# Performance work log

Hardware: AMD Instinct MI355X
Metric: run time of the kernel (lower is better)

## Reference

```python
import jax, jax.numpy as jnp
import numpy as np

IN_FEATURES = 4096
OUT_FEATURES = 11008
W_BITS = 4
GROUP_SIZE = 128
NUM_CHERRIES = 128                       # ceil(4096*0.03125)//8*8
NUM_NORMAL = IN_FEATURES - NUM_CHERRIES  # 3968
N_GROUPS = NUM_NORMAL // GROUP_SIZE      # 31
QROWS = NUM_NORMAL // 8 * W_BITS         # 1984 packed uint8 rows
QMIN = -(2 ** (W_BITS - 1))              # signed int4 min = -8
BATCH = 64


def setup_inputs() -> dict:
    key = jax.random.key(0)
    k1, k2, k3, k4, k5 = jax.random.split(key, 5)
    x = jax.random.normal(k1, (BATCH, IN_FEATURES), jnp.float32)
    # packed 4-bit weights: two nibbles per uint8, stored as [QROWS, out]
    qweight = jax.random.randint(k2, (QROWS, OUT_FEATURES), 0, 256, jnp.int32).astype(jnp.uint8)
    # per-group scales, stored transposed as [n_groups, out]
    scales = jax.random.uniform(k3, (N_GROUPS, OUT_FEATURES), jnp.float32, 0.005, 0.02)
    # full-precision outlier ('cherry') columns, stored as [num_cherries, out]
    cherry_weight = jax.random.normal(k4, (NUM_CHERRIES, OUT_FEATURES), jnp.float32) * 0.02
    rng = np.random.default_rng(0)
    cherry_indices = jnp.asarray(
        np.sort(rng.choice(IN_FEATURES, NUM_CHERRIES, replace=False)).astype(np.int32))
    bias = jax.random.normal(k5, (OUT_FEATURES,), jnp.float32) * 0.01
    return {"x": x, "qweight": qweight, "cherry_weight": cherry_weight,
            "cherry_indices": cherry_indices, "scales": scales, "bias": bias}


def _normal_indices(cherry_indices):
    # complement of cherry_indices, as in the torch scatter/nonzero construction
    mask = jnp.ones((IN_FEATURES,), dtype=bool).at[cherry_indices].set(False)
    return jnp.nonzero(mask, size=NUM_NORMAL)[0]  # static size -> jit ok


def reference(x, qweight, cherry_weight, cherry_indices, scales, bias):
    # --- unpack 4-bit weights (matches QuantLinear.unpack for w_bits=4) ---
    q = qweight.T                                    # [out, QROWS]
    nib = jnp.stack([q & 0xF, (q >> 4) & 0xF], axis=-1)  # low nibble first
    nib = nib.reshape(OUT_FEATURES, NUM_NORMAL)
    intw = nib.astype(jnp.int32) + QMIN              # signed int4 values
    # --- dequantize: repeat-interleave per-group scales along in dim ---
    s = jnp.repeat(scales.T, GROUP_SIZE, axis=1)     # [out, NUM_NORMAL]
    w_normal = intw.astype(s.dtype) * s              # dequantized normal weight
    # --- merge cherry outlier columns via column-gather on x (same math as
    #     scattering into a full [out, in] weight then x @ W.T) ---
    normal_idx = _normal_indices(cherry_indices)
    out = x[:, normal_idx] @ w_normal.T + x[:, cherry_indices] @ cherry_weight
    return out + bias
```

## Files before the change

### kernel.cpp

```cpp
#include <hip/hip_runtime.h>
#include <hip/hip_bf16.h>
#include <stdint.h>

#define IN_F 4096
#define OUT_F 11008
#define NUM_CH 128
#define NUM_NORM 3968
#define BATCH 64
#define KSPLIT 8
#define KCHUNK (IN_F / KSPLIT)
#define NMEGA (KCHUNK / 128)
#define BS 136

typedef short short8 __attribute__((ext_vector_type(8)));
typedef float float4v __attribute__((ext_vector_type(4)));
typedef int int4v __attribute__((ext_vector_type(4)));

__device__ __forceinline__ unsigned short f2bf(float f) {
    union { float f; unsigned u; } v; v.f = f;
    unsigned u = v.u;
    return (unsigned short)((u + 0x7FFFu + ((u >> 16) & 1u)) >> 16);
}

__device__ __forceinline__ unsigned pk_bf16(float lo, float hi) {
    __hip_bfloat162 h = __float22bfloat162_rn(make_float2(lo, hi));
    union { __hip_bfloat162 h; unsigned u; } c; c.h = h; return c.u;
}

__global__ __launch_bounds__(256) void init_out(
        const float* __restrict__ bias, float* __restrict__ out) {
    const int i = blockIdx.x * 256 + threadIdx.x;
    const int c = i % (OUT_F / 4);
    const float4v b4 = *reinterpret_cast<const float4v*>(bias + c * 4);
    reinterpret_cast<float4v*>(out)[i] = b4;
}

__global__ __launch_bounds__(256) void permute_x(
        const float* __restrict__ x, const int* __restrict__ cidx,
        unsigned short* __restrict__ xp) {
    int i = blockIdx.x * blockDim.x + threadIdx.x;
    int b = blockIdx.y;
    int lo = 0, hi = NUM_CH;
    while (lo < hi) { int mid = (lo + hi) >> 1; if (cidx[mid] < i) lo = mid + 1; else hi = mid; }
    bool isch = (lo < NUM_CH) && (cidx[lo] == i);
    int pos = isch ? (NUM_NORM + lo) : (i - lo);
    xp[b * IN_F + pos] = f2bf(x[b * IN_F + i]);
}

__global__ __launch_bounds__(256, 4) void qgemm(
        const unsigned short* __restrict__ xp, const int* __restrict__ qw,
        const float* __restrict__ cw, const float* __restrict__ scales,
        float* __restrict__ out) {
    __shared__ unsigned short Bt[2][64][BS];

    const int tid  = threadIdx.x;
    const int wave = tid >> 6;
    const int lane = tid & 63;
    const int ln   = lane & 15;
    const int lq   = lane >> 4;
    const int n0    = blockIdx.x * 64;
    const int kbase = blockIdx.y * KCHUNK;
    const int tcol = (tid & 15) << 2;
    const int trow = tid >> 4;

    const int*   qbase = qw + n0 + tcol;
    const float* sbase = scales + n0 + tcol;
    const float* cbase = cw + n0 + tcol;

    float4v acc[4];
    #pragma unroll
    for (int s = 0; s < 4; ++s) acc[s] = (float4v){0.f, 0.f, 0.f, 0.f};

    int4v qcur[4]; float4v scur;
    {
        const int rb = (kbase >> 1) + 4 * trow;
        #pragma unroll
        for (int i = 0; i < 4; ++i)
            qcur[i] = *reinterpret_cast<const int4v*>(qbase + (size_t)(rb + i) * OUT_F);
        scur = *reinterpret_cast<const float4v*>(sbase + (size_t)(kbase >> 7) * OUT_F);
    }

    for (int s = 0; s < NMEGA; ++s) {
        const int k0 = kbase + s * 128;
        unsigned short (*buf)[BS] = Bt[s & 1];

        if (k0 < NUM_NORM) {
            const int4v q0 = qcur[0], q1 = qcur[1], q2 = qcur[2], q3 = qcur[3];
            const float4v sc = scur;
            const int kn = k0 + 128;
            if (s + 1 < NMEGA && kn < NUM_NORM) {
                const int rb = (kn >> 1) + 4 * trow;
                #pragma unroll
                for (int i = 0; i < 4; ++i)
                    qcur[i] = *reinterpret_cast<const int4v*>(qbase + (size_t)(rb + i) * OUT_F);
                scur = *reinterpret_cast<const float4v*>(sbase + (size_t)(kn >> 7) * OUT_F);
            }
            const int4v qq[4] = {q0, q1, q2, q3};
            #pragma unroll
            for (int cc = 0; cc < 4; ++cc) {
                union { short8 v; unsigned u[4]; } wv;
                const float s1 = sc[cc];
                #pragma unroll
                for (int i = 0; i < 4; ++i) {
                    const int q = qq[i][cc];
                    wv.u[i] = pk_bf16((float)((q & 0xF) - 8) * s1,
                                      (float)(((q >> 4) & 0xF) - 8) * s1);
                }
                *reinterpret_cast<short8*>(&buf[tcol + cc][trow * 8]) = wv.v;
            }
        } else {
            float4v ch[8];
            #pragma unroll
            for (int j = 0; j < 8; ++j)
                ch[j] = *reinterpret_cast<const float4v*>(
                    cbase + (size_t)(8 * trow + j) * OUT_F);
            #pragma unroll
            for (int cc = 0; cc < 4; ++cc) {
                union { short8 v; unsigned u[4]; } wv;
                #pragma unroll
                for (int m = 0; m < 4; ++m)
                    wv.u[m] = pk_bf16(ch[2 * m][cc], ch[2 * m + 1][cc]);
                *reinterpret_cast<short8*>(&buf[tcol + cc][trow * 8]) = wv.v;
            }
        }

        __syncthreads();

        const unsigned short* xprow =
            xp + (size_t)((wave << 4) + ln) * IN_F + k0 + (lq << 3);
        const short8 a0 = *reinterpret_cast<const short8*>(xprow);
        const short8 a1 = *reinterpret_cast<const short8*>(xprow + 32);
        const short8 a2 = *reinterpret_cast<const short8*>(xprow + 64);
        const short8 a3 = *reinterpret_cast<const short8*>(xprow + 96);

        #pragma unroll
        for (int st = 0; st < 4; ++st) {
            const unsigned short* bp = &buf[(st << 4) + ln][lq << 3];
            acc[st] = __builtin_amdgcn_mfma_f32_16x16x32_bf16(
                a0, *reinterpret_cast<const short8*>(bp), acc[st], 0, 0, 0);
            acc[st] = __builtin_amdgcn_mfma_f32_16x16x32_bf16(
                a1, *reinterpret_cast<const short8*>(bp + 32), acc[st], 0, 0, 0);
            acc[st] = __builtin_amdgcn_mfma_f32_16x16x32_bf16(
                a2, *reinterpret_cast<const short8*>(bp + 64), acc[st], 0, 0, 0);
            acc[st] = __builtin_amdgcn_mfma_f32_16x16x32_bf16(
                a3, *reinterpret_cast<const short8*>(bp + 96), acc[st], 0, 0, 0);
        }
    }

    #pragma unroll
    for (int st = 0; st < 4; ++st) {
        const int n = n0 + (st << 4) + ln;
        #pragma unroll
        for (int r = 0; r < 4; ++r) {
            const int m = (wave << 4) + (lq << 2) + r;
            atomicAdd(&out[(size_t)m * OUT_F + n], acc[st][r]);
        }
    }
}

extern "C" void kernel_launch(void* const* d_in, const int* in_sizes, int n_in,
                              void* d_out, int out_size, void* d_ws, size_t ws_size,
                              hipStream_t stream) {
    const float* x      = (const float*)d_in[0];
    const int*   qw     = (const int*)d_in[1];
    const float* cw     = (const float*)d_in[2];
    const int*   cidx   = (const int*)d_in[3];
    const float* scales = (const float*)d_in[4];
    const float* bias   = (const float*)d_in[5];
    float*       out    = (float*)d_out;
    unsigned short* xp  = (unsigned short*)d_ws;

    init_out<<<(BATCH * OUT_F / 4) / 256, 256, 0, stream>>>(bias, out);
    dim3 pgrid(IN_F / 256, BATCH);
    permute_x<<<pgrid, 256, 0, stream>>>(x, cidx, xp);
    qgemm<<<dim3(OUT_F / 64, KSPLIT), 256, 0, stream>>>(xp, qw, cw, scales, out);
}
```

Before: 164.2 us.

## Give each wave a private 32-column weight tile and drop block barrier

Restructures the GEMM so each wave dequantizes and consumes its own 32-column slice of the weight tile in LDS, which removes the __syncthreads between the dequantize and MFMA phases. Each wave now covers all 64 batch rows times 32 columns, so the block spans 128 output columns and the grid halves along N. Activation fragments are prefetched one sub-step ahead of the MFMAs. In exchange, register pressure rises from more accumulators and prefetch buffers, and the launch-bounds hint drops from 4 to 3 blocks per SM. Activation rows are also re-read from global by every wave.

Result: slower. 174.8 us (+6.4%).

```diff
diff --git a/kernel.cpp b/kernel.cpp
--- a/kernel.cpp
+++ b/kernel.cpp
@@ -47,113 +47,134 @@
     xp[b * IN_F + pos] = f2bf(x[b * IN_F + i]);
 }
 
-__global__ __launch_bounds__(256, 4) void qgemm(
+__global__ __launch_bounds__(256, 3) void qgemm(
         const unsigned short* __restrict__ xp, const int* __restrict__ qw,
         const float* __restrict__ cw, const float* __restrict__ scales,
         float* __restrict__ out) {
-    __shared__ unsigned short Bt[2][64][BS];
+    __shared__ unsigned short Bt[4][32][BS];
 
     const int tid  = threadIdx.x;
     const int wave = tid >> 6;
     const int lane = tid & 63;
     const int ln   = lane & 15;
     const int lq   = lane >> 4;
-    const int n0    = blockIdx.x * 64;
+    const int c4   = (lane & 7) * 4;
+    const int rg   = lane >> 3;
+
+    const int n0w   = (blockIdx.x * 4 + wave) * 32;
     const int kbase = blockIdx.y * KCHUNK;
-    const int tcol = (tid & 15) << 2;
-    const int trow = tid >> 4;
 
-    const int*   qbase = qw + n0 + tcol;
-    const float* sbase = scales + n0 + tcol;
-    const float* cbase = cw + n0 + tcol;
+    unsigned short (*tile)[BS] = Bt[wave];
 
-    float4v acc[4];
+    const int*   qcolp = qw + n0w + c4;
+    const float* scolp = scales + n0w + c4;
+    const float* ccolp = cw + n0w + c4;
+
+    float4v acc[4][2];
     #pragma unroll
-    for (int s = 0; s < 4; ++s) acc[s] = (float4v){0.f, 0.f, 0.f, 0.f};
+    for (int mt = 0; mt < 4; ++mt)
+        #pragma unroll
+        for (int nf = 0; nf < 2; ++nf) acc[mt][nf] = (float4v){0.f, 0.f, 0.f, 0.f};
 
-    int4v qcur[4]; float4v scur;
+    int4v qcur[8]; float4v scur;
     {
-        const int rb = (kbase >> 1) + 4 * trow;
+        const size_t rb = (size_t)(kbase >> 1) + rg * 8;
         #pragma unroll
-        for (int i = 0; i < 4; ++i)
-            qcur[i] = *reinterpret_cast<const int4v*>(qbase + (size_t)(rb + i) * OUT_F);
-        scur = *reinterpret_cast<const float4v*>(sbase + (size_t)(kbase >> 7) * OUT_F);
+        for (int i = 0; i < 8; ++i)
+            qcur[i] = *reinterpret_cast<const int4v*>(qcolp + (rb + i) * OUT_F);
+        scur = *reinterpret_cast<const float4v*>(scolp + (size_t)(kbase >> 7) * OUT_F);
     }
 
     for (int s = 0; s < NMEGA; ++s) {
         const int k0 = kbase + s * 128;
-        unsigned short (*buf)[BS] = Bt[s & 1];
 
         if (k0 < NUM_NORM) {
-            const int4v q0 = qcur[0], q1 = qcur[1], q2 = qcur[2], q3 = qcur[3];
-            const float4v sc = scur;
+            int4v q[8]; const float4v sc = scur;
+            #pragma unroll
+            for (int i = 0; i < 8; ++i) q[i] = qcur[i];
             const int kn = k0 + 128;
             if (s + 1 < NMEGA && kn < NUM_NORM) {
-                const int rb = (kn >> 1) + 4 * trow;
+                const size_t rb = (size_t)(kn >> 1) + rg * 8;
                 #pragma unroll
-                for (int i = 0; i < 4; ++i)
-                    qcur[i] = *reinterpret_cast<const int4v*>(qbase + (size_t)(rb + i) * OUT_F);
-                scur = *reinterpret_cast<const float4v*>(sbase + (size_t)(kn >> 7) * OUT_F);
+                for (int i = 0; i < 8; ++i)
+                    qcur[i] = *reinterpret_cast<const int4v*>(qcolp + (rb + i) * OUT_F);
+                scur = *reinterpret_cast<const float4v*>(scolp + (size_t)(kn >> 7) * OUT_F);
             }
-            const int4v qq[4] = {q0, q1, q2, q3};
             #pragma unroll
-            for (int cc = 0; cc < 4; ++cc) {
-                union { short8 v; unsigned u[4]; } wv;
-                const float s1 = sc[cc];
+            for (int j = 0; j < 4; ++j) {
+                const float s1 = sc[j];
                 #pragma unroll
-                for (int i = 0; i < 4; ++i) {
-                    const int q = qq[i][cc];
-                    wv.u[i] = pk_bf16((float)((q & 0xF) - 8) * s1,
-                                      (float)(((q >> 4) & 0xF) - 8) * s1);
+                for (int p = 0; p < 2; ++p) {
+                    union { short8 v; unsigned u[4]; } wv;
+                    #pragma unroll
+                    for (int m = 0; m < 4; ++m) {
+                        const int qq = q[p * 4 + m][j];
+                        wv.u[m] = pk_bf16((float)((qq & 0xF) - 8) * s1,
+                                          (float)(((qq >> 4) & 0xF) - 8) * s1);
+                    }
+                    *reinterpret_cast<short8*>(&tile[c4 + j][rg * 16 + p * 8]) = wv.v;
                 }
-                *reinterpret_cast<short8*>(&buf[tcol + cc][trow * 8]) = wv.v;
             }
         } else {
-            float4v ch[8];
+            float4v chv[16];
             #pragma unroll
-            for (int j = 0; j < 8; ++j)
-                ch[j] = *reinterpret_cast<const float4v*>(
-                    cbase + (size_t)(8 * trow + j) * OUT_F);
+            for (int t = 0; t < 16; ++t)
+                chv[t] = *reinterpret_cast<const float4v*>(
+                    ccolp + (size_t)(rg * 16 + t) * OUT_F);
             #pragma unroll
-            for (int cc = 0; cc < 4; ++cc) {
-                union { short8 v; unsigned u[4]; } wv;
+            for (int j = 0; j < 4; ++j) {
                 #pragma unroll
-                for (int m = 0; m < 4; ++m)
-                    wv.u[m] = pk_bf16(ch[2 * m][cc], ch[2 * m + 1][cc]);
-                *reinterpret_cast<short8*>(&buf[tcol + cc][trow * 8]) = wv.v;
+                for (int p = 0; p < 2; ++p) {
+                    union { short8 v; unsigned u[4]; } wv;
+                    #pragma unroll
+                    for (int m = 0; m < 4; ++m)
+                        wv.u[m] = pk_bf16(chv[p * 8 + 2 * m][j], chv[p * 8 + 2 * m + 1][j]);
+                    *reinterpret_cast<short8*>(&tile[c4 + j][rg * 16 + p * 8]) = wv.v;
+                }
             }
         }
 
-        __syncthreads();
-
-        const unsigned short* xprow =
-            xp + (size_t)((wave << 4) + ln) * IN_F + k0 + (lq << 3);
-        const short8 a0 = *reinterpret_cast<const short8*>(xprow);
-        const short8 a1 = *reinterpret_cast<const short8*>(xprow + 32);
-        const short8 a2 = *reinterpret_cast<const short8*>(xprow + 64);
-        const short8 a3 = *reinterpret_cast<const short8*>(xprow + 96);
+        short8 a_sub[4];
+        #pragma unroll
+        for (int mt = 0; mt < 4; ++mt)
+            a_sub[mt] = *reinterpret_cast<const short8*>(
+                xp + (size_t)(mt * 16 + ln) * IN_F + k0 + (lq << 3));
 
         #pragma unroll
-        for (int st = 0; st < 4; ++st) {
-            const unsigned short* bp = &buf[(st << 4) + ln][lq << 3];
-            acc[st] = __builtin_amdgcn_mfma_f32_16x16x32_bf16(
-                a0, *reinterpret_cast<const short8*>(bp), acc[st], 0, 0, 0);
-            acc[st] = __builtin_amdgcn_mfma_f32_16x16x32_bf16(
-                a1, *reinterpret_cast<const short8*>(bp + 32), acc[st], 0, 0, 0);
-            acc[st] = __builtin_amdgcn_mfma_f32_16x16x32_bf16(
-                a2, *reinterpret_cast<const short8*>(bp + 64), acc[st], 0, 0, 0);
-            acc[st] = __builtin_amdgcn_mfma_f32_16x16x32_bf16(
-                a3, *reinterpret_cast<const short8*>(bp + 96), acc[st], 0, 0, 0);
+        for (int sub = 0; sub < 4; ++sub) {
+            const short8 b0 = *reinterpret_cast<const short8*>(
+                &tile[ln][sub * 32 + (lq << 3)]);
+            const short8 b1 = *reinterpret_cast<const short8*>(
+                &tile[16 + ln][sub * 32 + (lq << 3)]);
+            short8 a_nxt[4];
+            if (sub < 3) {
+                #pragma unroll
+                for (int mt = 0; mt < 4; ++mt)
+                    a_nxt[mt] = *reinterpret_cast<const short8*>(
+                        xp + (size_t)(mt * 16 + ln) * IN_F + k0 + (sub + 1) * 32 + (lq << 3));
+            }
+            #pragma unroll
+            for (int mt = 0; mt < 4; ++mt) {
+                acc[mt][0] = __builtin_amdgcn_mfma_f32_16x16x32_bf16(a_sub[mt], b0, acc[mt][0], 0, 0, 0);
+                acc[mt][1] = __builtin_amdgcn_mfma_f32_16x16x32_bf16(a_sub[mt], b1, acc[mt][1], 0, 0, 0);
+            }
+            if (sub < 3) {
+                #pragma unroll
+                for (int mt = 0; mt < 4; ++mt) a_sub[mt] = a_nxt[mt];
+            }
         }
     }
 
     #pragma unroll
-    for (int st = 0; st < 4; ++st) {
-        const int n = n0 + (st << 4) + ln;
+    for (int mt = 0; mt < 4; ++mt) {
         #pragma unroll
-        for (int r = 0; r < 4; ++r) {
-            const int m = (wave << 4) + (lq << 2) + r;
-            atomicAdd(&out[(size_t)m * OUT_F + n], acc[st][r]);
+        for (int nf = 0; nf < 2; ++nf) {
+            const int n = n0w + nf * 16 + ln;
+            #pragma unroll
+            for (int r = 0; r < 4; ++r) {
+                const int m = mt * 16 + (lq << 2) + r;
+                atomicAdd(&out[(size_t)m * OUT_F + n], acc[mt][nf][r]);
+            }
         }
     }
 }
@@ -173,5 +194,5 @@
     init_out<<<(BATCH * OUT_F / 4) / 256, 256, 0, stream>>>(bias, out);
     dim3 pgrid(IN_F / 256, BATCH);
     permute_x<<<pgrid, 256, 0, stream>>>(x, cidx, xp);
-    qgemm<<<dim3(OUT_F / 64, KSPLIT), 256, 0, stream>>>(xp, qw, cw, scales, out);
+    qgemm<<<dim3(OUT_F / 128, KSPLIT), 256, 0, stream>>>(xp, qw, cw, scales, out);
 }
```
